# Optimization experiments

Measured on AMD Instinct MI355X. Metric: run time of the kernel, lower is better.

Reference implementation:

```python
import jax, jax.numpy as jnp
import numpy as np

IN_CH = 64
OUT_CH = 64
SEQ_LEN = 2048
MODES = 64  # modes2 = min(modes1, seq_len//2) = 64
SCALE = 1.0 / (IN_CH * OUT_CH)


def setup_inputs() -> dict:
    key = jax.random.key(0)
    k1, k2, k3 = jax.random.split(key, 3)
    x = jax.random.normal(k1, (32, 8, IN_CH, SEQ_LEN), dtype=jnp.float32)
    # torch.rand(...) complex init scaled by 1/(in*out): real & imag in [0, scale)
    wr = SCALE * jax.random.uniform(k2, (IN_CH, OUT_CH, MODES), dtype=jnp.float32)
    wi = SCALE * jax.random.uniform(k3, (IN_CH, OUT_CH, MODES), dtype=jnp.float32)
    return {"x": x, "wr": wr, "wi": wi}


def reference(x, wr, wi):
    # x: [B, H, E, N] real; weights complex [in, out, modes]
    N = x.shape[-1]
    w = jax.lax.complex(wr, wi)
    x_ft = jnp.fft.rfft(x)                       # [B, H, E, N//2+1] complex64
    a = x_ft[..., :MODES]                        # keep only low modes
    out_low = jnp.einsum('bjix,iox->bjox', a, w)  # per-mode complex matmul
    # zero-fill remaining frequency bins (equivalent to out_ft zeros + slice set)
    pad = N // 2 + 1 - MODES
    out_ft = jnp.pad(out_low, ((0, 0), (0, 0), (0, 0), (0, pad)))
    return jnp.fft.irfft(out_ft, n=N)            # [B, H, out_ch, N] real
```

## Files before the change

kernel.cpp:

```cpp
#include <hip/hip_runtime.h>
#include <hip/hip_bf16.h>


typedef __bf16 bf16x8 __attribute__((ext_vector_type(8)));
typedef float  f32x4  __attribute__((ext_vector_type(4)));

#define SEQ 2048
#define NM2 128

__device__ __forceinline__ unsigned int rnbf(float f) {
  unsigned int u = __builtin_bit_cast(unsigned int, f);
  return (u + 0x7fffu + ((u >> 16) & 1u)) >> 16;
}
__device__ __forceinline__ unsigned int pack2(float a, float b) {
  return rnbf(a) | (rnbf(b) << 16);
}
__device__ __forceinline__ float frombf(unsigned int lo16_in_place) {
  return __builtin_bit_cast(float, lo16_in_place);
}

typedef const __attribute__((address_space(1))) unsigned int gu32;
typedef __attribute__((address_space(3))) unsigned int lu32;

__global__ __launch_bounds__(256) void k_tables(unsigned short* __restrict__ t1sw,
                                                unsigned short* __restrict__ t2t) {
  int idx = blockIdx.x * 256 + threadIdx.x;
  int k = idx >> 11;
  int n = idx & 2047;
  float rev = (float)((k * n) & 2047) * (1.0f / 2048.0f);
  float s, co;
  asm("v_sin_f32 %0, %1" : "=v"(s)  : "v"(rev));
  asm("v_cos_f32 %0, %1" : "=v"(co) : "v"(rev));
  float ck = (k == 0 ? 1.0f : 2.0f) * (1.0f / 2048.0f);
  int kt = n >> 6, part = (n >> 3) & 7, e = n & 7;
  unsigned base = (unsigned)kt * 16384u + 2u * (unsigned)e;
  unsigned offc = base + (((unsigned)(k * 128 + part * 16)) ^ (((unsigned)k & 7u) << 4));
  int c2 = k + 64;
  unsigned offs = base + (((unsigned)(c2 * 128 + part * 16)) ^ (((unsigned)c2 & 7u) << 4));
  *(unsigned short*)((char*)t1sw + offc) = (unsigned short)rnbf(co);
  *(unsigned short*)((char*)t1sw + offs) = (unsigned short)rnbf(-s);
  t2t[n * NM2 + k]      = (unsigned short)rnbf(ck * co);
  t2t[n * NM2 + k + 64] = (unsigned short)rnbf(-ck * s);
}

__global__ __launch_bounds__(256) void k_gemm1(const float* __restrict__ x,
                                               const unsigned short* __restrict__ t1sw,
                                               unsigned short* __restrict__ A) {
  __shared__ int4 lds4[49152 / 16];
  char* lds = (char*)lds4;
  const int tid = threadIdx.x, wave = tid >> 6, lane = tid & 63;
  const int r0 = blockIdx.x * 32;

  const float* xsrc[2];
#pragma unroll
  for (int p = 0; p < 2; ++p) {
    const int row = p * 16 + wave * 4 + (lane >> 4);
    const int u = (lane & 15) ^ (row & 7);
    xsrc[p] = x + (size_t)(r0 + row) * SEQ + u * 4;
  }

  f32x4 acc[4] = {};

#pragma unroll
  for (int p = 0; p < 2; ++p)
    __builtin_amdgcn_global_load_lds((gu32*)(xsrc[p]),
                                     (lu32*)(lds + p * 4096 + wave * 1024), 16, 0, 0);
#pragma unroll
  for (int p = 0; p < 4; ++p)
    __builtin_amdgcn_global_load_lds((gu32*)((const char*)t1sw + (p * 256 + tid) * 16),
                                     (lu32*)(lds + 16384 + p * 4096 + wave * 1024), 16, 0, 0);
  asm volatile("s_waitcnt vmcnt(0)" ::: "memory");
  __builtin_amdgcn_s_barrier();

  const int wr = wave >> 1, wc = wave & 1;
  const int a = wr * 16 + (lane & 15);
  const unsigned xra = (unsigned)(a & 7) << 4;
  const int kg = lane >> 4;

  for (int it = 0; it < 32; ++it) {
    const int cur = it & 1, nxt = cur ^ 1;
    const int xoff = cur * 8192;
    const int toff = 16384 + cur * 16384;
    if (it < 31) {
      const char* tg = (const char*)t1sw + (size_t)(it + 1) * 16384;
#pragma unroll
      for (int p = 0; p < 2; ++p)
        __builtin_amdgcn_global_load_lds((gu32*)(xsrc[p] + (it + 1) * 64),
                                         (lu32*)(lds + nxt * 8192 + p * 4096 + wave * 1024),
                                         16, 0, 0);
#pragma unroll
      for (int p = 0; p < 4; ++p)
        __builtin_amdgcn_global_load_lds((gu32*)(tg + (p * 256 + tid) * 16),
                                         (lu32*)(lds + 16384 + nxt * 16384 + p * 4096 + wave * 1024),
                                         16, 0, 0);
    }
#pragma unroll
    for (int kss = 0; kss < 2; ++kss) {
      const unsigned byte0 = (unsigned)(a * 256 + kss * 128 + kg * 32);
      const f32x4 lo = *(const f32x4*)(lds + xoff + (byte0 ^ xra));
      const f32x4 hi = *(const f32x4*)(lds + xoff + ((byte0 + 16) ^ xra));
      unsigned c0, c1, c2, c3;
      asm("v_cvt_pk_bf16_f32 %0, %1, %2" : "=v"(c0) : "v"(lo[0]), "v"(lo[1]));
      asm("v_cvt_pk_bf16_f32 %0, %1, %2" : "=v"(c1) : "v"(lo[2]), "v"(lo[3]));
      asm("v_cvt_pk_bf16_f32 %0, %1, %2" : "=v"(c2) : "v"(hi[0]), "v"(hi[1]));
      asm("v_cvt_pk_bf16_f32 %0, %1, %2" : "=v"(c3) : "v"(hi[2]), "v"(hi[3]));
      uint4 pk; pk.x = c0; pk.y = c1; pk.z = c2; pk.w = c3;
      const bf16x8 av = __builtin_bit_cast(bf16x8, pk);
#pragma unroll
      for (int t = 0; t < 4; ++t) {
        const int col = wc * 64 + t * 16 + (lane & 15);
        const bf16x8 bv = *(const bf16x8*)(lds + toff +
            ((col * 128 + kss * 64 + kg * 16) ^ ((unsigned)(col & 7) << 4)));
        acc[t] = __builtin_amdgcn_mfma_f32_16x16x32_bf16(bv, av, acc[t], 0, 0, 0);
      }
    }
    asm volatile("s_waitcnt vmcnt(0)" ::: "memory");
    __builtin_amdgcn_s_barrier();
  }
  const int row = r0 + wr * 16 + (lane & 15);
#pragma unroll
  for (int t = 0; t < 4; ++t) {
    const int col0 = wc * 64 + t * 16 + kg * 4;
    uint2 v; v.x = pack2(acc[t][0], acc[t][1]); v.y = pack2(acc[t][2], acc[t][3]);
    *(uint2*)(A + (size_t)row * NM2 + col0) = v;
  }
}

__global__ __launch_bounds__(256) void k_stage2(const unsigned short* __restrict__ A,
                                                const float* __restrict__ wr,
                                                const float* __restrict__ wi,
                                                unsigned short* __restrict__ Bx) {
  __shared__ float sA[2][64][64];
  const int b = blockIdx.x;
  const int bjc = b >> 2, oh = (b >> 1) & 1, kh = b & 1;
  const int k0 = kh * 32;
  const int tid = threadIdx.x;
#pragma unroll
  for (int p = 0; p < 8; ++p) {
    int fidx = tid + 256 * p;
    int row = fidx >> 4, q = fidx & 15;
    int colbf = (q < 8) ? (k0 + q * 4) : (64 + k0 + (q - 8) * 4);
    uint2 u = *(const uint2*)(A + (size_t)(bjc * 128 + row) * NM2 + colbf);
    f32x4 v;
    v[0] = frombf(u.x << 16);
    v[1] = frombf(u.x & 0xffff0000u);
    v[2] = frombf(u.y << 16);
    v[3] = frombf(u.y & 0xffff0000u);
    int dcol = (q < 8) ? q * 4 : 32 + (q - 8) * 4;
    *(f32x4*)(&sA[row >> 6][row & 63][dcol]) = v;
  }
  __syncthreads();
  const int o = oh * 32 + (tid >> 3);
  const int kg = tid & 7;
  const int kb = k0 + kg * 4;
  f32x4 accr[2] = {};
  f32x4 acci[2] = {};
  for (int i = 0; i < 64; ++i) {
    f32x4 wrv = *(const f32x4*)(wr + (i * 64 + o) * 64 + kb);
    f32x4 wiv = *(const f32x4*)(wi + (i * 64 + o) * 64 + kb);
#pragma unroll
    for (int bj = 0; bj < 2; ++bj) {
      f32x4 ar = *(const f32x4*)(&sA[bj][i][kg * 4]);
      f32x4 ai = *(const f32x4*)(&sA[bj][i][32 + kg * 4]);
#pragma unroll
      for (int kk = 0; kk < 4; ++kk) {
        accr[bj][kk] += ar[kk] * wrv[kk] - ai[kk] * wiv[kk];
        acci[bj][kk] += ar[kk] * wiv[kk] + ai[kk] * wrv[kk];
      }
    }
  }
#pragma unroll
  for (int bj = 0; bj < 2; ++bj) {
    const int r = (bjc * 2 + bj) * 64 + o;
    uint2 vr; vr.x = pack2(accr[bj][0], accr[bj][1]); vr.y = pack2(accr[bj][2], accr[bj][3]);
    uint2 vi; vi.x = pack2(acci[bj][0], acci[bj][1]); vi.y = pack2(acci[bj][2], acci[bj][3]);
    *(uint2*)(Bx + (size_t)r * NM2 + kb)      = vr;
    *(uint2*)(Bx + (size_t)r * NM2 + 64 + kb) = vi;
  }
}

__global__ __launch_bounds__(256) void k_gemm2(const unsigned short* __restrict__ Bx,
                                               const unsigned short* __restrict__ t2t,
                                               float* __restrict__ out) {
  __shared__ int4 lds4[65536 / 16];
  char* lds = (char*)lds4;
  const int tid = threadIdx.x, wave = tid >> 6, lane = tid & 63;
  const int swz = (blockIdx.x & 7) * 256 + (blockIdx.x >> 3);
  const int mb = swz >> 4, nb = swz & 15;
  const int r0 = mb * 128, n0 = nb * 128;
#pragma unroll
  for (int p = 0; p < 8; ++p) {
    int seg = tid + 256 * p;
    int row = seg >> 4, part = seg & 15;
    unsigned sw = (unsigned)((row * 256 + part * 16) ^ ((row & 7) << 4));
    int4 va = *(const int4*)(Bx + (size_t)(r0 + row) * NM2 + part * 8);
    *(int4*)(lds + sw) = va;
    int4 vb = *(const int4*)(t2t + (size_t)(n0 + row) * NM2 + part * 8);
    *(int4*)(lds + 32768 + sw) = vb;
  }
  __syncthreads();
  f32x4 acc[2][8] = {};
#pragma unroll
  for (int ks = 0; ks < 4; ++ks) {
    const int ar0 = wave * 32 + (lane & 15);
    const int ar1 = ar0 + 16;
    const int koff = ks * 64 + (lane >> 4) * 16;
    bf16x8 a0 = *(const bf16x8*)(lds + ((ar0 * 256 + koff) ^ ((unsigned)(ar0 & 7) << 4)));
    bf16x8 a1 = *(const bf16x8*)(lds + ((ar1 * 256 + koff) ^ ((unsigned)(ar1 & 7) << 4)));
#pragma unroll
    for (int t = 0; t < 8; ++t) {
      const int col = t * 16 + (lane & 15);
      bf16x8 bv = *(const bf16x8*)(lds + 32768 + ((col * 256 + koff) ^ ((unsigned)(col & 7) << 4)));
      acc[0][t] = __builtin_amdgcn_mfma_f32_16x16x32_bf16(bv, a0, acc[0][t], 0, 0, 0);
      acc[1][t] = __builtin_amdgcn_mfma_f32_16x16x32_bf16(bv, a1, acc[1][t], 0, 0, 0);
    }
  }
#pragma unroll
  for (int m = 0; m < 2; ++m) {
    const int row = r0 + wave * 32 + m * 16 + (lane & 15);
#pragma unroll
    for (int t = 0; t < 8; ++t) {
      const int col = n0 + t * 16 + (lane >> 4) * 4;
      *(f32x4*)(out + (size_t)row * SEQ + col) = acc[m][t];
    }
  }
}

extern "C" void kernel_launch(void* const* d_in, const int* in_sizes, int n_in,
                              void* d_out, int out_size, void* d_ws, size_t ws_size,
                              hipStream_t stream) {
  const float* x  = (const float*)d_in[0];
  const float* wr = (const float*)d_in[1];
  const float* wi = (const float*)d_in[2];
  float* out = (float*)d_out;
  char* ws = (char*)d_ws;
  unsigned short* t1sw = (unsigned short*)(ws);
  unsigned short* t2t  = (unsigned short*)(ws + 524288);
  unsigned short* A    = (unsigned short*)(ws + 1048576);
  unsigned short* Bx   = (unsigned short*)(ws + 1048576 + (size_t)16384 * NM2 * 2);

  k_tables<<<dim3(512),  dim3(256), 0, stream>>>(t1sw, t2t);
  k_gemm1 <<<dim3(512),  dim3(256), 0, stream>>>(x, t1sw, A);
  k_stage2<<<dim3(512),  dim3(256), 0, stream>>>(A, wr, wi, Bx);
  k_gemm2 <<<dim3(2048), dim3(256), 0, stream>>>(Bx, t2t, out);
}
```

Measured before the change: 105.8 us.

## Split-K the forward DFT GEMM with 64-row tiles and triple-buffered x staging

The forward DFT GEMM now uses 64-row tiles, so each table tile staged in LDS is reused across twice as many rows. The K dimension is split in two across blocks so the grid stays at 512 blocks. x is triple-buffered with a partial vmcnt wait, overlapping loads with MFMA better. The two bf16 partial results are written separately and summed in stage2. This adds an extra bf16 rounding of the partials and another workspace read, and raises LDS use to 80KB, which limits occupancy.

```diff
diff --git a/kernel.cpp b/kernel.cpp
--- a/kernel.cpp
+++ b/kernel.cpp
@@ -7,6 +7,7 @@
 
 #define SEQ 2048
 #define NM2 128
+#define KS  2
 
 __device__ __forceinline__ unsigned int rnbf(float f) {
   unsigned int u = __builtin_bit_cast(unsigned int, f);
@@ -45,55 +46,60 @@
 
 __global__ __launch_bounds__(256) void k_gemm1(const float* __restrict__ x,
                                                const unsigned short* __restrict__ t1sw,
-                                               unsigned short* __restrict__ A) {
-  __shared__ int4 lds4[49152 / 16];
+                                               unsigned short* __restrict__ P) {
+  __shared__ int4 lds4[81920 / 16];
   char* lds = (char*)lds4;
   const int tid = threadIdx.x, wave = tid >> 6, lane = tid & 63;
-  const int r0 = blockIdx.x * 32;
-
-  const float* xsrc[2];
-#pragma unroll
-  for (int p = 0; p < 2; ++p) {
+  const int mtile = blockIdx.x >> 1, ks = blockIdx.x & (KS - 1);
+  const int r0 = mtile * 64;
+  const int kbase = ks * (SEQ / KS);
+  const char* t1base = (const char*)t1sw + (size_t)(kbase >> 6) * 16384;
+
+  const float* xsrc[4];
+#pragma unroll
+  for (int p = 0; p < 4; ++p) {
     const int row = p * 16 + wave * 4 + (lane >> 4);
     const int u = (lane & 15) ^ (row & 7);
-    xsrc[p] = x + (size_t)(r0 + row) * SEQ + u * 4;
-  }
-
-  f32x4 acc[4] = {};
-
-#pragma unroll
-  for (int p = 0; p < 2; ++p)
-    __builtin_amdgcn_global_load_lds((gu32*)(xsrc[p]),
-                                     (lu32*)(lds + p * 4096 + wave * 1024), 16, 0, 0);
-#pragma unroll
-  for (int p = 0; p < 4; ++p)
-    __builtin_amdgcn_global_load_lds((gu32*)((const char*)t1sw + (p * 256 + tid) * 16),
-                                     (lu32*)(lds + 16384 + p * 4096 + wave * 1024), 16, 0, 0);
-  asm volatile("s_waitcnt vmcnt(0)" ::: "memory");
-  __builtin_amdgcn_s_barrier();
-
-  const int wr = wave >> 1, wc = wave & 1;
-  const int a = wr * 16 + (lane & 15);
+    xsrc[p] = x + (size_t)(r0 + row) * SEQ + kbase + u * 4;
+  }
+
+#define STAGE_X(t, buf)                                                              \
+  {                                                                                  \
+    _Pragma("unroll")                                                                \
+    for (int p = 0; p < 4; ++p)                                                      \
+      __builtin_amdgcn_global_load_lds((gu32*)(xsrc[p] + (t) * 64),                  \
+          (lu32*)(lds + (buf) * 16384 + p * 4096 + wave * 1024), 16, 0, 0);          \
+  }
+#define STAGE_T(t, buf)                                                              \
+  {                                                                                  \
+    const char* tg_ = t1base + (size_t)(t) * 16384;                                  \
+    _Pragma("unroll")                                                                \
+    for (int p = 0; p < 4; ++p)                                                      \
+      __builtin_amdgcn_global_load_lds((gu32*)(tg_ + (p * 256 + tid) * 16),          \
+          (lu32*)(lds + 49152 + (buf) * 16384 + p * 4096 + wave * 1024), 16, 0, 0);  \
+  }
+
+  f32x4 acc[8] = {};
+
+  STAGE_T(0, 0);
+  STAGE_X(0, 0);
+  STAGE_X(1, 1);
+
+  const int a = wave * 16 + (lane & 15);
   const unsigned xra = (unsigned)(a & 7) << 4;
   const int kg = lane >> 4;
 
-  for (int it = 0; it < 32; ++it) {
-    const int cur = it & 1, nxt = cur ^ 1;
-    const int xoff = cur * 8192;
-    const int toff = 16384 + cur * 16384;
-    if (it < 31) {
-      const char* tg = (const char*)t1sw + (size_t)(it + 1) * 16384;
-#pragma unroll
-      for (int p = 0; p < 2; ++p)
-        __builtin_amdgcn_global_load_lds((gu32*)(xsrc[p] + (it + 1) * 64),
-                                         (lu32*)(lds + nxt * 8192 + p * 4096 + wave * 1024),
-                                         16, 0, 0);
-#pragma unroll
-      for (int p = 0; p < 4; ++p)
-        __builtin_amdgcn_global_load_lds((gu32*)(tg + (p * 256 + tid) * 16),
-                                         (lu32*)(lds + 16384 + nxt * 16384 + p * 4096 + wave * 1024),
-                                         16, 0, 0);
-    }
+  for (int it = 0; it < 16; ++it) {
+    asm volatile("s_waitcnt vmcnt(4)" ::: "memory");
+    __builtin_amdgcn_s_barrier();
+    {
+      const int tn = (it + 1 < 16) ? it + 1 : 15;
+      const int xn = (it + 2 < 16) ? it + 2 : 15;
+      STAGE_T(tn, (it + 1) & 1);
+      STAGE_X(xn, (it + 2) % 3);
+    }
+    const int xoff = (it % 3) * 16384;
+    const int toff = 49152 + (it & 1) * 16384;
 #pragma unroll
     for (int kss = 0; kss < 2; ++kss) {
       const unsigned byte0 = (unsigned)(a * 256 + kss * 128 + kg * 32);
@@ -107,26 +113,27 @@
       uint4 pk; pk.x = c0; pk.y = c1; pk.z = c2; pk.w = c3;
       const bf16x8 av = __builtin_bit_cast(bf16x8, pk);
 #pragma unroll
-      for (int t = 0; t < 4; ++t) {
-        const int col = wc * 64 + t * 16 + (lane & 15);
+      for (int t = 0; t < 8; ++t) {
+        const int col = t * 16 + (lane & 15);
         const bf16x8 bv = *(const bf16x8*)(lds + toff +
             ((col * 128 + kss * 64 + kg * 16) ^ ((unsigned)(col & 7) << 4)));
         acc[t] = __builtin_amdgcn_mfma_f32_16x16x32_bf16(bv, av, acc[t], 0, 0, 0);
       }
     }
-    asm volatile("s_waitcnt vmcnt(0)" ::: "memory");
-    __builtin_amdgcn_s_barrier();
-  }
-  const int row = r0 + wr * 16 + (lane & 15);
-#pragma unroll
-  for (int t = 0; t < 4; ++t) {
-    const int col0 = wc * 64 + t * 16 + kg * 4;
+  }
+  unsigned short* Pout = P + (size_t)ks * (16384 * NM2);
+  const int row = r0 + wave * 16 + (lane & 15);
+#pragma unroll
+  for (int t = 0; t < 8; ++t) {
+    const int col0 = t * 16 + kg * 4;
     uint2 v; v.x = pack2(acc[t][0], acc[t][1]); v.y = pack2(acc[t][2], acc[t][3]);
-    *(uint2*)(A + (size_t)row * NM2 + col0) = v;
-  }
-}
-
-__global__ __launch_bounds__(256) void k_stage2(const unsigned short* __restrict__ A,
+    *(uint2*)(Pout + (size_t)row * NM2 + col0) = v;
+  }
+#undef STAGE_X
+#undef STAGE_T
+}
+
+__global__ __launch_bounds__(256) void k_stage2(const unsigned short* __restrict__ P,
                                                 const float* __restrict__ wr,
                                                 const float* __restrict__ wi,
                                                 unsigned short* __restrict__ Bx) {
@@ -140,12 +147,14 @@
     int fidx = tid + 256 * p;
     int row = fidx >> 4, q = fidx & 15;
     int colbf = (q < 8) ? (k0 + q * 4) : (64 + k0 + (q - 8) * 4);
-    uint2 u = *(const uint2*)(A + (size_t)(bjc * 128 + row) * NM2 + colbf);
+    const unsigned short* base = P + (size_t)(bjc * 128 + row) * NM2 + colbf;
+    uint2 u0 = *(const uint2*)(base);
+    uint2 u1 = *(const uint2*)(base + (size_t)16384 * NM2);
     f32x4 v;
-    v[0] = frombf(u.x << 16);
-    v[1] = frombf(u.x & 0xffff0000u);
-    v[2] = frombf(u.y << 16);
-    v[3] = frombf(u.y & 0xffff0000u);
+    v[0] = frombf(u0.x << 16)         + frombf(u1.x << 16);
+    v[1] = frombf(u0.x & 0xffff0000u) + frombf(u1.x & 0xffff0000u);
+    v[2] = frombf(u0.y << 16)         + frombf(u1.y << 16);
+    v[3] = frombf(u0.y & 0xffff0000u) + frombf(u1.y & 0xffff0000u);
     int dcol = (q < 8) ? q * 4 : 32 + (q - 8) * 4;
     *(f32x4*)(&sA[row >> 6][row & 63][dcol]) = v;
   }
@@ -236,11 +245,11 @@
   char* ws = (char*)d_ws;
   unsigned short* t1sw = (unsigned short*)(ws);
   unsigned short* t2t  = (unsigned short*)(ws + 524288);
-  unsigned short* A    = (unsigned short*)(ws + 1048576);
-  unsigned short* Bx   = (unsigned short*)(ws + 1048576 + (size_t)16384 * NM2 * 2);
-
-  k_tables<<<dim3(512),  dim3(256), 0, stream>>>(t1sw, t2t);
-  k_gemm1 <<<dim3(512),  dim3(256), 0, stream>>>(x, t1sw, A);
-  k_stage2<<<dim3(512),  dim3(256), 0, stream>>>(A, wr, wi, Bx);
-  k_gemm2 <<<dim3(2048), dim3(256), 0, stream>>>(Bx, t2t, out);
-}
+  unsigned short* P    = (unsigned short*)(ws + 1048576);
+  unsigned short* Bx   = (unsigned short*)(ws + 1048576 + (size_t)KS * 16384 * NM2 * 2);
+
+  k_tables<<<dim3(512),      dim3(256), 0, stream>>>(t1sw, t2t);
+  k_gemm1 <<<dim3(256 * KS), dim3(256), 0, stream>>>(x, t1sw, P);
+  k_stage2<<<dim3(512),      dim3(256), 0, stream>>>(P, wr, wi, Bx);
+  k_gemm2 <<<dim3(2048),     dim3(256), 0, stream>>>(Bx, t2t, out);
+}
```

Result: faster. 99.01 us (-6.4%).
